# Performance work log

Hardware: AMD Instinct MI355X
Metric: run time of the kernel (lower is better)

Reference implementation:

```python
import jax, jax.numpy as jnp
import numpy as np
from jax import lax

KERNEL = 3
CIN = 512
FMAPS = 512
LATENT = 512
GAIN = 1.0
LRMUL = 1.0
# StyleGAN2 wscale: runtime_coef = gain / sqrt(fan_in) * lrmul
RC_W = GAIN / np.sqrt(KERNEL * KERNEL * CIN) * LRMUL
RC_S = GAIN / np.sqrt(LATENT) * LRMUL


def setup_inputs() -> dict:
    key = jax.random.key(0)
    k1, k2, k3, k4, k5 = jax.random.split(key, 5)
    N, H, W = 8, 64, 64
    x = jax.random.normal(k1, (N, CIN, H, W), dtype=jnp.float32)
    dlatent_vect = jax.random.normal(k2, (N, LATENT), dtype=jnp.float32)
    weight = jax.random.normal(k3, (KERNEL, KERNEL, CIN, FMAPS), dtype=jnp.float32)
    mod_weight = jax.random.normal(k4, (LATENT, CIN), dtype=jnp.float32)
    mod_bias = jax.random.normal(k5, (CIN,), dtype=jnp.float32)
    return {"x": x, "dlatent_vect": dlatent_vect, "weight": weight,
            "mod_weight": mod_weight, "mod_bias": mod_bias}


def reference(x, dlatent_vect, weight, mod_weight, mod_bias):
    N, _, H, W = x.shape
    w = weight * RC_W                                       # [kh,kw,Cin,Cout]
    # style: s = A(dlatent) + 1
    s = dlatent_vect @ (mod_weight * RC_S) + mod_bias * LRMUL + 1.0  # [N,Cin]
    # per-sample modulated weights
    ww = w[None] * s[:, None, None, :, None]                # [N,kh,kw,Cin,Cout]
    # demodulate
    d = lax.rsqrt(jnp.sum(jnp.square(ww), axis=(1, 2, 3)) + 1e-8)  # [N,Cout]
    ww = ww * d[:, None, None, None, :]
    # fused modconv: one grouped conv with N groups
    xr = x.reshape(1, N * CIN, H, W)
    wr = jnp.transpose(ww, (1, 2, 3, 0, 4)).reshape(KERNEL, KERNEL, CIN, N * FMAPS)
    out = lax.conv_general_dilated(
        xr, wr, window_strides=(1, 1), padding="SAME",
        dimension_numbers=("NCHW", "HWIO", "NCHW"),
        feature_group_count=N)
    return out.reshape(N, FMAPS, H, W)
```

## Files before the change

### kernel.cpp

```cpp
#include <hip/hip_runtime.h>
#include <math.h>

#define CIN_    512
#define COUT_   512
#define LATENT_ 512
#define NB_     8
#define HH_     64
#define WW_     64

typedef float f32x16 __attribute__((ext_vector_type(16)));
typedef short bf16x8v __attribute__((ext_vector_type(8)));

__device__ inline unsigned short f2bf(float f) {
    union { float f; unsigned u; } v; v.f = f;
    unsigned r = v.u + 0x7fffu + ((v.u >> 16) & 1u);
    return (unsigned short)(r >> 16);
}

__device__ __forceinline__ void gl_lds16(const void* g, void* l) {
    __builtin_amdgcn_global_load_lds(
        (const __attribute__((address_space(1))) unsigned int*)g,
        (__attribute__((address_space(3))) unsigned int*)l,
        16, 0, 0);
}

__global__ __launch_bounds__(256) void prep1(
    const float* __restrict__ w, const float* __restrict__ dlat,
    const float* __restrict__ mw, const float* __restrict__ mb,
    float* __restrict__ wsq, unsigned short* __restrict__ wb,
    float* __restrict__ s)
{
    __shared__ float smem[16 * 521];
    const float RC_W = 0.0147313912747197f;
    const float RC_S = 0.0441941738241592f;
    int b = blockIdx.x;
    int t = threadIdx.x;

    if (b < 1024) {
        int idx = b * 256 + t;
        float acc = 0.f;
#pragma unroll
        for (int tap = 0; tap < 9; ++tap) {
            float v = w[tap * (CIN_ * COUT_) + idx];
            acc += v * v;
        }
        wsq[idx] = acc;
    } else if (b < 1312) {
        int bb  = b - 1024;
        int tap = bb / 32;
        int cb  = bb % 32;
        for (int idx = t; idx < 16 * 512; idx += 256) {
            int ci = idx >> 9;
            int co = idx & 511;
            smem[ci * 521 + co] = w[((size_t)tap * 512 + cb * 16 + ci) * 512 + co];
        }
        __syncthreads();
        unsigned short* dst = wb + (size_t)(tap * 32 + cb) * 1024 * 8;
        for (int p = t; p < 2048; p += 256) {
            int l  = (p >> 1) & 63;
            int g  = p >> 7;
            int co = g * 32 + (l & 31);
            int ci = (l >> 5) * 8 + (p & 1) * 4;
            ushort4 o4;
            o4.x = f2bf(smem[(ci + 0) * 521 + co] * RC_W);
            o4.y = f2bf(smem[(ci + 1) * 521 + co] * RC_W);
            o4.z = f2bf(smem[(ci + 2) * 521 + co] * RC_W);
            o4.w = f2bf(smem[(ci + 3) * 521 + co] * RC_W);
            *(ushort4*)&dst[p * 4] = o4;
        }
    } else {
        int bb  = b - 1312;
        int n   = bb >> 3;
        int ci0 = (bb & 7) * 64;
        for (int i = t; i < LATENT_; i += 256) smem[i] = dlat[n * LATENT_ + i];
        __syncthreads();
        int cil  = t & 63;
        int part = t >> 6;
        const float* mwp = mw + ci0 + cil;
        float a0 = 0.f, a1 = 0.f;
        int l0 = part * 128;
#pragma unroll 4
        for (int l = l0; l < l0 + 128; l += 2) {
            a0 += smem[l]     * mwp[(size_t)l * CIN_];
            a1 += smem[l + 1] * mwp[(size_t)(l + 1) * CIN_];
        }
        smem[512 + part * 64 + cil] = a0 + a1;
        __syncthreads();
        if (t < 64) {
            float r = smem[512 + t] + smem[576 + t] + smem[640 + t] + smem[704 + t];
            s[n * CIN_ + ci0 + t] = r * RC_S + mb[ci0 + t] + 1.0f;
        }
    }
}

__global__ __launch_bounds__(256) void prep2(
    const float* __restrict__ x, const float* __restrict__ s,
    const float* __restrict__ wsq, float* __restrict__ dmod,
    unsigned short* __restrict__ xt)
{
    __shared__ float smem[16 * 67 + 16];
    int b = blockIdx.x;
    int t = threadIdx.x;

    if (b < 64) {
        const float RCW2 = 1.0f / 4608.0f;
        int n   = b >> 3;
        int co0 = (b & 7) * 64;
        for (int i = t; i < CIN_; i += 256) { float v = s[n * CIN_ + i]; smem[i] = v * v; }
        __syncthreads();
        int col  = t & 63;
        int part = t >> 6;
        const float* wp = wsq + co0 + col;
        float a0 = 0.f, a1 = 0.f;
        int c0 = part * 128;
#pragma unroll 4
        for (int ci = c0; ci < c0 + 128; ci += 2) {
            a0 += smem[ci]     * wp[(size_t)ci * COUT_];
            a1 += smem[ci + 1] * wp[(size_t)(ci + 1) * COUT_];
        }
        smem[512 + part * 64 + col] = a0 + a1;
        __syncthreads();
        if (t < 64) {
            float r = smem[512 + t] + smem[576 + t] + smem[640 + t] + smem[704 + t];
            dmod[n * COUT_ + co0 + t] = rsqrtf(RCW2 * r + 1e-8f);
        }
    } else {
        int bb = b - 64;
        int rg = bb % 6;
        int cb = (bb / 6) % 32;
        int n  = bb / (6 * 32);

        if (t < 16) smem[16 * 67 + t] = s[n * CIN_ + cb * 16 + t];

        for (int hp = rg * 11; hp < rg * 11 + 11; ++hp) {
            int gh = hp - 1;
            bool rowok = (gh >= 0) && (gh < HH_);
            if (rowok) {
                const float* src = &x[(((size_t)n * CIN_ + cb * 16) * HH_ + gh) * WW_];
                int ci = t >> 4;
                int g0 = (t & 15) * 4;
                float4 v = *(const float4*)&src[(size_t)ci * (HH_ * WW_) + g0];
                float* dstl = &smem[ci * 67 + g0];
                dstl[0] = v.x; dstl[1] = v.y; dstl[2] = v.z; dstl[3] = v.w;
            }
            __syncthreads();

            unsigned short* dst = xt + (((size_t)(n * 32 + cb) * 66 + hp) * 66) * 16;
            for (int p = t; p < 264; p += 256) {
                int e   = p * 4;
                int wp_ = e >> 4;
                int cie = e & 15;
                int gw  = wp_ - 1;
                float vv0 = 0.f, vv1 = 0.f, vv2 = 0.f, vv3 = 0.f;
                if (rowok && gw >= 0 && gw < WW_) {
                    vv0 = smem[(cie + 0) * 67 + gw] * smem[16 * 67 + cie + 0];
                    vv1 = smem[(cie + 1) * 67 + gw] * smem[16 * 67 + cie + 1];
                    vv2 = smem[(cie + 2) * 67 + gw] * smem[16 * 67 + cie + 2];
                    vv3 = smem[(cie + 3) * 67 + gw] * smem[16 * 67 + cie + 3];
                }
                ushort4 o4;
                o4.x = f2bf(vv0); o4.y = f2bf(vv1); o4.z = f2bf(vv2); o4.w = f2bf(vv3);
                *(ushort4*)&dst[e] = o4;
            }
            __syncthreads();
        }
    }
}

__global__ __launch_bounds__(256, 2) void conv_mfma(
    const unsigned short* __restrict__ xt,
    const unsigned short* __restrict__ wb,
    const float* __restrict__ dmod,
    float* __restrict__ out)
{
    __shared__ __align__(16) union {
        struct {
            unsigned short xs[2][512 * 8];
            unsigned short ws[3][4096];
        } s;
        float o[64 * 129];
    } sm;

    int b   = blockIdx.x;
    int cot = b & 1;
    int wt_ = (b >> 1) & 3;
    int ht  = (b >> 3) & 7;
    int n   = b >> 6;
    int h0 = ht * 8, w0 = wt_ * 16, co0 = cot * 256;

    int t    = threadIdx.x;
    int wv   = t >> 6, lane = t & 63;
    int mh   = wv >> 1, nh = wv & 1;
    int l5   = lane & 31, half = lane >> 5;

    const int wsrc0 = t * 8, wsrc1 = (t + 256) * 8;
    const int wdst0 = (t & ~63) * 8, wdst1 = ((t + 256) & ~63) * 8;
    int m0 = t ^ ((t >> 3) & 7);
    int li1 = t + 256;
    int m1 = li1 ^ ((li1 >> 3) & 7); if (m1 > 359) m1 = 359;
    const int xsrc0 = (m0 / 36) * 1056 + (m0 % 36) * 8;
    const int xsrc1 = (m1 / 36) * 1056 + (m1 % 36) * 8;
    const int xdst0 = (t & ~63) * 8, xdst1 = ((t + 256) & ~63) * 8;

    f32x16 acc[2][4];
#pragma unroll
    for (int ms = 0; ms < 2; ++ms)
#pragma unroll
        for (int ns = 0; ns < 4; ++ns)
#pragma unroll
            for (int i = 0; i < 16; ++i) acc[ms][ns][i] = 0.f;

    auto stage_ws = [&](int cb2, int tap2, int q) {
        const unsigned short* tsrc = wb + ((size_t)(tap2 * 32 + cb2) * 1024 + cot * 512) * 8;
        unsigned short* d = (unsigned short*)sm.s.ws[q];
        gl_lds16(&tsrc[wsrc0], &d[wdst0]);
        gl_lds16(&tsrc[wsrc1], &d[wdst1]);
    };
    auto stage_xs = [&](int cb2, int bq) {
        const unsigned short* xb2 = xt + (((size_t)(n * 32 + cb2) * 66 + h0) * 66 + w0) * 16;
        unsigned short* d = (unsigned short*)sm.s.xs[bq];
        gl_lds16(&xb2[xsrc0], &d[xdst0]);
        gl_lds16(&xb2[xsrc1], &d[xdst1]);
    };

    stage_ws(0, 0, 0);
    stage_ws(0, 1, 1);
    stage_xs(0, 0);
    asm volatile("s_waitcnt vmcnt(0)" ::: "memory");
    __builtin_amdgcn_s_barrier();

    for (int cb = 0; cb < 32; ++cb) {
        const unsigned short* xsb = (const unsigned short*)sm.s.xs[cb & 1];
#pragma unroll
        for (int tap = 0; tap < 9; ++tap) {
            const int p  = tap % 3;
            const int q2 = (tap + 2) % 3;
            const int kh = tap / 3, kw = tap % 3;

            bf16x8v bfr[4], afr[2];
            const unsigned short* wsb = (const unsigned short*)sm.s.ws[p];
#pragma unroll
            for (int ns = 0; ns < 4; ++ns)
                bfr[ns] = *(const bf16x8v*)&wsb[((nh * 4 + ns) * 64 + lane) * 8];
#pragma unroll
            for (int ms = 0; ms < 2; ++ms) {
                int pr = mh * 4 + ms * 2 + (l5 >> 4);
                int pc = l5 & 15;
                int pos = (pr + kh) * 18 + (pc + kw);
                int ch  = pos * 2 + half;
                ch ^= (ch >> 3) & 7;
                afr[ms] = *(const bf16x8v*)&xsb[ch * 8];
            }

            {
                int tap2 = tap + 2, cb2 = cb;
                if (tap2 >= 9) { tap2 -= 9; cb2 = cb + 1; }
                if (cb2 > 31) cb2 = 31;
                stage_ws(cb2, tap2, q2);
            }
            if (tap == 4) {
                int cb2 = (cb + 1 > 31) ? 31 : cb + 1;
                stage_xs(cb2, (cb + 1) & 1);
            }

            __builtin_amdgcn_s_setprio(1);
#pragma unroll
            for (int ms = 0; ms < 2; ++ms)
#pragma unroll
                for (int ns = 0; ns < 4; ++ns)
                    acc[ms][ns] = __builtin_amdgcn_mfma_f32_32x32x16_bf16(
                        afr[ms], bfr[ns], acc[ms][ns], 0, 0, 0);
            __builtin_amdgcn_s_setprio(0);

            if (tap == 4) asm volatile("s_waitcnt vmcnt(4)" ::: "memory");
            else          asm volatile("s_waitcnt vmcnt(2)" ::: "memory");
            __builtin_amdgcn_s_barrier();
        }
    }

    asm volatile("s_waitcnt vmcnt(0)" ::: "memory");

    for (int pss = 0; pss < 4; ++pss) {
        __syncthreads();
        if (nh == (pss >> 1)) {
#pragma unroll
            for (int q = 0; q < 2; ++q) {
                int bco = q * 32 + l5;
                float dv = dmod[n * COUT_ + co0 + pss * 64 + bco];
#pragma unroll
                for (int ms = 0; ms < 2; ++ms) {
#pragma unroll
                    for (int reg = 0; reg < 16; ++reg) {
                        int ml = (reg & 3) + 8 * (reg >> 2) + 4 * half;
                        int m  = mh * 64 + ms * 32 + ml;
                        sm.o[bco * 129 + m] = acc[ms][(pss & 1) * 2 + q][reg] * dv;
                    }
                }
            }
        }
        __syncthreads();
        for (int j = t; j < 2048; j += 256) {
            int wq = j & 3;
            int pairidx = j >> 2;
            int row  = pairidx & 7;
            int bco2 = pairidx >> 3;
            int co = co0 + pss * 64 + bco2;
            const float* src = &sm.o[bco2 * 129 + row * 16 + wq * 4];
            float4 v = make_float4(src[0], src[1], src[2], src[3]);
            *(float4*)&out[(((size_t)n * COUT_ + co) * HH_ + h0 + row) * WW_ + w0 + wq * 4] = v;
        }
    }
}

extern "C" void kernel_launch(void* const* d_in, const int* in_sizes, int n_in,
                              void* d_out, int out_size, void* d_ws, size_t ws_size,
                              hipStream_t stream) {
    const float* x    = (const float*)d_in[0];
    const float* dlat = (const float*)d_in[1];
    const float* w    = (const float*)d_in[2];
    const float* mw   = (const float*)d_in[3];
    const float* mb   = (const float*)d_in[4];
    float* out = (float*)d_out;

    char* ws = (char*)d_ws;
    float* s    = (float*)(ws);
    float* dmod = (float*)(ws + 16384);
    float* wsq  = (float*)(ws + 32768);
    unsigned short* xt = (unsigned short*)(ws + 1081344);
    unsigned short* wb = (unsigned short*)(ws + 36765696);

    prep1<<<1376, 256, 0, stream>>>(w, dlat, mw, mb, wsq, wb, s);
    prep2<<<64 + NB_ * 32 * 6, 256, 0, stream>>>(x, s, wsq, dmod, xt);
    conv_mfma<<<512, 256, 0, stream>>>(xt, wb, dmod, out);
}
```

Measured before the change: 257.4 us.

## Stage weights three taps at a time with double-buffered LDS

The conv main loop now loads weights for a whole kernel row (three taps) per stage into two alternating LDS buffers, replacing the three-slot per-tap ring. This cuts barriers from nine to three per channel block and puts more MFMA work between them. The cost is more LDS (weights grow from 24KB to 48KB) and a full __syncthreads drain each stage, which may lower occupancy and expose more load latency. Separately, the prep kernel's x loader prefetches the next row into registers before the current row is written to shared memory.

```diff
diff --git a/kernel.cpp b/kernel.cpp
--- a/kernel.cpp
+++ b/kernel.cpp
@@ -132,14 +132,25 @@
 
         if (t < 16) smem[16 * 67 + t] = s[n * CIN_ + cb * 16 + t];
 
-        for (int hp = rg * 11; hp < rg * 11 + 11; ++hp) {
+        int ci = t >> 4;
+        int g0 = (t & 15) * 4;
+        const float* srcbase = &x[(((size_t)(n * CIN_ + cb * 16 + ci)) * HH_) * WW_ + g0];
+        int hp0 = rg * 11;
+
+        float4 v = make_float4(0.f, 0.f, 0.f, 0.f);
+        {
+            int gh = hp0 - 1;
+            if (gh >= 0 && gh < HH_) v = *(const float4*)&srcbase[(size_t)gh * WW_];
+        }
+        for (int hp = hp0; hp < hp0 + 11; ++hp) {
             int gh = hp - 1;
             bool rowok = (gh >= 0) && (gh < HH_);
+            float4 vn = make_float4(0.f, 0.f, 0.f, 0.f);
+            int ghn = gh + 1;
+            if ((hp + 1 < hp0 + 11) && ghn >= 0 && ghn < HH_)
+                vn = *(const float4*)&srcbase[(size_t)ghn * WW_];
+
             if (rowok) {
-                const float* src = &x[(((size_t)n * CIN_ + cb * 16) * HH_ + gh) * WW_];
-                int ci = t >> 4;
-                int g0 = (t & 15) * 4;
-                float4 v = *(const float4*)&src[(size_t)ci * (HH_ * WW_) + g0];
                 float* dstl = &smem[ci * 67 + g0];
                 dstl[0] = v.x; dstl[1] = v.y; dstl[2] = v.z; dstl[3] = v.w;
             }
@@ -163,6 +174,7 @@
                 *(ushort4*)&dst[e] = o4;
             }
             __syncthreads();
+            v = vn;
         }
     }
 }
@@ -176,7 +188,7 @@
     __shared__ __align__(16) union {
         struct {
             unsigned short xs[2][512 * 8];
-            unsigned short ws[3][4096];
+            unsigned short ws[2][3 * 512 * 8];
         } s;
         float o[64 * 129];
     } sm;
@@ -210,75 +222,74 @@
 #pragma unroll
             for (int i = 0; i < 16; ++i) acc[ms][ns][i] = 0.f;
 
-    auto stage_ws = [&](int cb2, int tap2, int q) {
-        const unsigned short* tsrc = wb + ((size_t)(tap2 * 32 + cb2) * 1024 + cot * 512) * 8;
-        unsigned short* d = (unsigned short*)sm.s.ws[q];
-        gl_lds16(&tsrc[wsrc0], &d[wdst0]);
-        gl_lds16(&tsrc[wsrc1], &d[wdst1]);
+    auto stage_tri = [&](int cb2, int j2, unsigned short* dbuf) {
+#pragma unroll
+        for (int tt = 0; tt < 3; ++tt) {
+            int tap2 = j2 * 3 + tt;
+            const unsigned short* tsrc =
+                wb + ((size_t)(tap2 * 32 + cb2) * 1024 + cot * 512) * 8;
+            gl_lds16(&tsrc[wsrc0], &dbuf[tt * 4096 + wdst0]);
+            gl_lds16(&tsrc[wsrc1], &dbuf[tt * 4096 + wdst1]);
+        }
     };
-    auto stage_xs = [&](int cb2, int bq) {
-        const unsigned short* xb2 = xt + (((size_t)(n * 32 + cb2) * 66 + h0) * 66 + w0) * 16;
-        unsigned short* d = (unsigned short*)sm.s.xs[bq];
-        gl_lds16(&xb2[xsrc0], &d[xdst0]);
-        gl_lds16(&xb2[xsrc1], &d[xdst1]);
+    auto stage_xs = [&](int cb2, unsigned short* dbuf) {
+        const unsigned short* xb2 =
+            xt + (((size_t)(n * 32 + cb2) * 66 + h0) * 66 + w0) * 16;
+        gl_lds16(&xb2[xsrc0], &dbuf[xdst0]);
+        gl_lds16(&xb2[xsrc1], &dbuf[xdst1]);
     };
 
-    stage_ws(0, 0, 0);
-    stage_ws(0, 1, 1);
-    stage_xs(0, 0);
-    asm volatile("s_waitcnt vmcnt(0)" ::: "memory");
-    __builtin_amdgcn_s_barrier();
+    unsigned short* wsR = (unsigned short*)sm.s.ws[0];
+    unsigned short* wsS = (unsigned short*)sm.s.ws[1];
+    unsigned short* xsR = (unsigned short*)sm.s.xs[0];
+    unsigned short* xsP = (unsigned short*)sm.s.xs[1];
+
+    stage_tri(0, 0, wsR);
+    stage_xs(0, xsR);
+    __syncthreads();
 
     for (int cb = 0; cb < 32; ++cb) {
-        const unsigned short* xsb = (const unsigned short*)sm.s.xs[cb & 1];
-#pragma unroll
-        for (int tap = 0; tap < 9; ++tap) {
-            const int p  = tap % 3;
-            const int q2 = (tap + 2) % 3;
-            const int kh = tap / 3, kw = tap % 3;
-
-            bf16x8v bfr[4], afr[2];
-            const unsigned short* wsb = (const unsigned short*)sm.s.ws[p];
-#pragma unroll
-            for (int ns = 0; ns < 4; ++ns)
-                bfr[ns] = *(const bf16x8v*)&wsb[((nh * 4 + ns) * 64 + lane) * 8];
-#pragma unroll
-            for (int ms = 0; ms < 2; ++ms) {
-                int pr = mh * 4 + ms * 2 + (l5 >> 4);
-                int pc = l5 & 15;
-                int pos = (pr + kh) * 18 + (pc + kw);
-                int ch  = pos * 2 + half;
-                ch ^= (ch >> 3) & 7;
-                afr[ms] = *(const bf16x8v*)&xsb[ch * 8];
-            }
-
-            {
-                int tap2 = tap + 2, cb2 = cb;
-                if (tap2 >= 9) { tap2 -= 9; cb2 = cb + 1; }
-                if (cb2 > 31) cb2 = 31;
-                stage_ws(cb2, tap2, q2);
-            }
-            if (tap == 4) {
-                int cb2 = (cb + 1 > 31) ? 31 : cb + 1;
-                stage_xs(cb2, (cb + 1) & 1);
+#pragma unroll
+        for (int j = 0; j < 3; ++j) {
+            int snext = cb * 3 + j + 1;
+            if (snext > 95) snext = 95;
+            stage_tri(snext / 3, snext % 3, wsS);
+            if (j == 1) {
+                int cbn = (cb + 1 > 31) ? 31 : cb + 1;
+                stage_xs(cbn, xsP);
             }
 
             __builtin_amdgcn_s_setprio(1);
 #pragma unroll
-            for (int ms = 0; ms < 2; ++ms)
+            for (int tt = 0; tt < 3; ++tt) {
+                bf16x8v bfr[4], afr[2];
+                const unsigned short* wsb = wsR + tt * 4096;
 #pragma unroll
                 for (int ns = 0; ns < 4; ++ns)
-                    acc[ms][ns] = __builtin_amdgcn_mfma_f32_32x32x16_bf16(
-                        afr[ms], bfr[ns], acc[ms][ns], 0, 0, 0);
+                    bfr[ns] = *(const bf16x8v*)&wsb[((nh * 4 + ns) * 64 + lane) * 8];
+#pragma unroll
+                for (int ms = 0; ms < 2; ++ms) {
+                    int pr = mh * 4 + ms * 2 + (l5 >> 4);
+                    int pc = l5 & 15;
+                    int pos = (pr + j) * 18 + (pc + tt);
+                    int ch  = pos * 2 + half;
+                    ch ^= (ch >> 3) & 7;
+                    afr[ms] = *(const bf16x8v*)&xsR[ch * 8];
+                }
+#pragma unroll
+                for (int ms = 0; ms < 2; ++ms)
+#pragma unroll
+                    for (int ns = 0; ns < 4; ++ns)
+                        acc[ms][ns] = __builtin_amdgcn_mfma_f32_32x32x16_bf16(
+                            afr[ms], bfr[ns], acc[ms][ns], 0, 0, 0);
+            }
             __builtin_amdgcn_s_setprio(0);
 
-            if (tap == 4) asm volatile("s_waitcnt vmcnt(4)" ::: "memory");
-            else          asm volatile("s_waitcnt vmcnt(2)" ::: "memory");
-            __builtin_amdgcn_s_barrier();
-        }
+            { unsigned short* tmp = wsR; wsR = wsS; wsS = tmp; }
+            __syncthreads();
+        }
+        { unsigned short* tmp = xsR; xsR = xsP; xsP = tmp; }
     }
-
-    asm volatile("s_waitcnt vmcnt(0)" ::: "memory");
 
     for (int pss = 0; pss < 4; ++pss) {
         __syncthreads();
@@ -299,9 +310,9 @@
             }
         }
         __syncthreads();
-        for (int j = t; j < 2048; j += 256) {
-            int wq = j & 3;
-            int pairidx = j >> 2;
+        for (int jj = t; jj < 2048; jj += 256) {
+            int wq = jj & 3;
+            int pairidx = jj >> 2;
             int row  = pairidx & 7;
             int bco2 = pairidx >> 3;
             int co = co0 + pss * 64 + bco2;
```

New measurement: 265.7 us. +3.2%, slower.
